# Performance work log

Hardware: AMD Instinct MI355X
Metric: run time of the kernel (lower is better)

Reference implementation:

```python
import jax, jax.numpy as jnp
import numpy as np

# dims
B, T, C, D, H, NH, HD, INTER, L = 4, 1024, 256, 256, 512, 8, 64, 2048, 4
CF, CB, BASE = 0, 128, 10000.0  # context_forward, context_backward, rope theta


def _rope_tables():
    inv = 1.0 / (BASE ** (jnp.arange(0, HD, 2, dtype=jnp.float32) / HD))
    t = jnp.arange(T, dtype=jnp.float32)
    f = jnp.einsum('i,j->ij', t, inv)          # [T, HD/2]
    emb = jnp.concatenate([f, f], axis=-1)      # [T, HD]
    return jnp.cos(emb), jnp.sin(emb)


def _rotate_half(x):
    x1, x2 = jnp.split(x, 2, axis=-1)
    return jnp.concatenate([-x2, x1], axis=-1)


def _ln(x, g, b):
    m = x.mean(-1, keepdims=True)
    v = ((x - m) ** 2).mean(-1, keepdims=True)
    return (x - m) / jnp.sqrt(v + 1e-5) * g + b


def _band_mask():
    # create_context_mask(CF, CB, T): allow j in [i-CB, i+CF]
    i = jnp.arange(T)[:, None]
    j = jnp.arange(T)[None, :]
    return (j <= i + CF) & (j >= i - CB)  # [T, T] bool


def setup_inputs() -> dict:
    key = jax.random.key(0)
    ks = jax.random.split(key, 16)
    w = lambda k, shp: (0.02 * jax.random.normal(k, shp)).astype(jnp.float32)
    return {
        'spikes': jax.random.normal(ks[0], (B, T, C), dtype=jnp.float32),
        'spikes_mask': jnp.ones((B, T), dtype=jnp.int32),
        'spikes_timestamp': jnp.tile(jnp.arange(T, dtype=jnp.int32), (B, 1)),
        'embed_w': w(ks[1], (C, D)), 'embed_b': jnp.zeros((D,), jnp.float32),
        'proj_w': w(ks[2], (D, H)), 'proj_b': jnp.zeros((H,), jnp.float32),
        'ln1_g': jnp.ones((L, H), jnp.float32), 'ln1_b': jnp.zeros((L, H), jnp.float32),
        'Wq': w(ks[3], (L, H, H)), 'bq': jnp.zeros((L, H), jnp.float32),
        'Wk': w(ks[4], (L, H, H)), 'bk': jnp.zeros((L, H), jnp.float32),
        'Wv': w(ks[5], (L, H, H)), 'bv': jnp.zeros((L, H), jnp.float32),
        'Wo': w(ks[6], (L, H, H)), 'bo': jnp.zeros((L, H), jnp.float32),
        'ln2_g': jnp.ones((L, H), jnp.float32), 'ln2_b': jnp.zeros((L, H), jnp.float32),
        'up_w': w(ks[7], (L, H, INTER)), 'up_b': jnp.zeros((L, INTER), jnp.float32),
        'down_w': w(ks[8], (L, INTER, H)), 'down_b': jnp.zeros((L, H), jnp.float32),
    }


def reference(spikes, spikes_mask, spikes_timestamp, embed_w, embed_b, proj_w, proj_b,
              ln1_g, ln1_b, Wq, bq, Wk, bk, Wv, bv, Wo, bo, ln2_g, ln2_b,
              up_w, up_b, down_w, down_b):
    cos, sin = _rope_tables()
    mask = _band_mask()[None, None] & (spikes_mask[:, None, None, :] > 0)  # [B,1,T,T]
    cs = cos[spikes_timestamp][:, None]  # [B,1,T,HD]
    sn = sin[spikes_timestamp][:, None]
    neg = jnp.finfo(jnp.float32).min

    # NeuralEmbeddingLayer (no stack/pos/tokens): Linear -> gelu -> Linear
    x = jax.nn.gelu(spikes @ embed_w + embed_b, approximate=False) @ proj_w + proj_b

    for l in range(L):
        h = _ln(x, ln1_g[l], ln1_b[l])
        q = (h @ Wq[l] + bq[l]).reshape(B, T, NH, HD).transpose(0, 2, 1, 3)
        k = (h @ Wk[l] + bk[l]).reshape(B, T, NH, HD).transpose(0, 2, 1, 3)
        v = (h @ Wv[l] + bv[l]).reshape(B, T, NH, HD).transpose(0, 2, 1, 3)
        q = q * cs + _rotate_half(q) * sn
        k = k * cs + _rotate_half(k) * sn
        s = jnp.einsum('bhqd,bhkd->bhqk', q, k) / np.float32(np.sqrt(HD))
        s = jnp.where(mask, s, neg)
        p = jax.nn.softmax(s, axis=-1)
        o = jnp.einsum('bhqk,bhkd->bhqd', p, v).transpose(0, 2, 1, 3).reshape(B, T, H)
        x = x + o @ Wo[l] + bo[l]
        h = _ln(x, ln2_g[l], ln2_b[l])
        x = x + jax.nn.gelu(h @ up_w[l] + up_b[l], approximate=False) @ down_w[l] + down_b[l]
    return x
```

## Files before the change

### kernel.cpp

```cpp
#include <hip/hip_runtime.h>
#include <math.h>

#define B_ 4
#define T_ 1024
#define C_ 256
#define D_ 256
#define H_ 512
#define NH_ 8
#define HD_ 64
#define INTER_ 2048
#define L_ 4
#define CB_ 128

typedef short bf16x8 __attribute__((ext_vector_type(8)));
typedef unsigned short ush8 __attribute__((ext_vector_type(8)));
typedef float f32x4 __attribute__((ext_vector_type(4)));

__device__ __forceinline__ float gelu_exact(float x) {
    return 0.5f * x * (1.0f + erff(x * 0.70710678118654752f));
}

__device__ __forceinline__ unsigned short f2bf(float f) {
    unsigned u = __float_as_uint(f);
    u += 0x7fffu + ((u >> 16) & 1u);
    return (unsigned short)(u >> 16);
}
__device__ __forceinline__ float bf2f(unsigned short h) {
    return __uint_as_float((unsigned)h << 16);
}

__device__ __forceinline__ void xcd_swz(int& bx, int& by) {
    const int gx  = gridDim.x;
    const int nwg = gx * gridDim.y;
    int bid = blockIdx.y * gx + blockIdx.x;
    bid = (bid & 7) * (nwg >> 3) + (bid >> 3);
    bx = bid % gx;
    by = bid / gx;
}

template<int ACT, int RES, int OBF, int SPLIT>
__global__ __launch_bounds__(256) void mm64_k(
    const unsigned short* __restrict__ A, const unsigned short* __restrict__ BT,
    const float* __restrict__ b0, const float* __restrict__ b1,
    const float* __restrict__ b2,
    const float* res,
    void* o0, void* o1, void* o2,
    const int M, const int N, const int K)
{
    __shared__ unsigned short As[2][64 * 64];
    __shared__ unsigned short Bs[2][64 * 64];

    int bx, by; xcd_swz(bx, by);

    const int tid  = threadIdx.x;
    const int lane = tid & 63;
    const int w    = tid >> 6;
    const int m0   = by * 64;
    const int n0   = bx * 64;
    const int wm   = (w >> 1) * 32;
    const int wn   = (w & 1) * 32;
    const int l16  = lane & 15;
    const int g16  = lane >> 4;

    f32x4 acc[2][2] = {};

    const unsigned short* Abase = A  + (size_t)m0 * K;
    const unsigned short* Bbase = BT + (size_t)n0 * K;

    const int c0 = (w << 6) + lane;
    const int c1 = c0 + 256;
    const int r0c = c0 >> 3, gk0 = (c0 & 7) ^ (r0c & 7);
    const int r1c = c1 >> 3, gk1 = (c1 & 7) ^ (r1c & 7);

#define STAGE64(buf, kk0) do {                                                                        \
    __builtin_amdgcn_global_load_lds(                                                                 \
        (const __attribute__((address_space(1))) unsigned*)(Abase + (size_t)r0c * K + (kk0) + gk0 * 8), \
        (__attribute__((address_space(3))) unsigned*)(As[buf] + (size_t)(w << 6) * 8), 16, 0, 0);     \
    __builtin_amdgcn_global_load_lds(                                                                 \
        (const __attribute__((address_space(1))) unsigned*)(Abase + (size_t)r1c * K + (kk0) + gk1 * 8), \
        (__attribute__((address_space(3))) unsigned*)(As[buf] + (size_t)(256 + (w << 6)) * 8), 16, 0, 0); \
    __builtin_amdgcn_global_load_lds(                                                                 \
        (const __attribute__((address_space(1))) unsigned*)(Bbase + (size_t)r0c * K + (kk0) + gk0 * 8), \
        (__attribute__((address_space(3))) unsigned*)(Bs[buf] + (size_t)(w << 6) * 8), 16, 0, 0);     \
    __builtin_amdgcn_global_load_lds(                                                                 \
        (const __attribute__((address_space(1))) unsigned*)(Bbase + (size_t)r1c * K + (kk0) + gk1 * 8), \
        (__attribute__((address_space(3))) unsigned*)(Bs[buf] + (size_t)(256 + (w << 6)) * 8), 16, 0, 0); \
} while (0)

    for (int k0 = 0; k0 < K; k0 += 128) {
        __syncthreads();
        STAGE64(0, k0);
        STAGE64(1, k0 + 64);
        __syncthreads();

#pragma unroll
        for (int half = 0; half < 2; ++half) {
#pragma unroll
            for (int kk = 0; kk < 2; ++kk) {
                const int kf = kk * 4 + g16;
                const int sw = (kf ^ (l16 & 7)) * 8;
                bf16x8 a[2], b[2];
#pragma unroll
                for (int t = 0; t < 2; ++t)
                    a[t] = *(const bf16x8*)&As[half][(wm + t * 16 + l16) * 64 + sw];
#pragma unroll
                for (int t = 0; t < 2; ++t)
                    b[t] = *(const bf16x8*)&Bs[half][(wn + t * 16 + l16) * 64 + sw];
#pragma unroll
                for (int i = 0; i < 2; ++i)
#pragma unroll
                    for (int j = 0; j < 2; ++j)
                        acc[i][j] = __builtin_amdgcn_mfma_f32_16x16x32_bf16(a[i], b[j], acc[i][j], 0, 0, 0);
            }
        }
    }
#undef STAGE64

    if (OBF || SPLIT) {
        __syncthreads();
        unsigned short* Eb = ((w < 2) ? As[0] : Bs[0]) + (w & 1) * 1024;
        const int row16 = lane >> 2;
        const int cg    = lane & 3;

        const int gnb   = n0 + wn;
        const int which = SPLIT ? (gnb >> 9) : 0;
        const int lnb   = SPLIT ? (gnb & 511) : gnb;
        const int ldo   = SPLIT ? 512 : N;
        unsigned short* oo = SPLIT
            ? ((which == 0) ? (unsigned short*)o0 : (which == 1) ? (unsigned short*)o1 : (unsigned short*)o2)
            : (unsigned short*)o0;
        const float* bb = SPLIT ? ((which == 0) ? b0 : (which == 1) ? b1 : b2) : b0;
        const float scale = (SPLIT && which == 0) ? 0.125f : 1.0f;

#pragma unroll
        for (int i = 0; i < 2; ++i) {
#pragma unroll
            for (int j = 0; j < 2; ++j) {
                const float bv = bb[lnb + j * 16 + l16];
#pragma unroll
                for (int r = 0; r < 4; ++r) {
                    float cv = acc[i][j][r] + bv;
                    if (ACT) cv = gelu_exact(cv);
                    if (SPLIT) cv *= scale;
                    Eb[(g16 * 4 + r) * 40 + j * 16 + l16] = f2bf(cv);
                }
            }
            const int grow0 = m0 + wm + i * 16 + row16;
#pragma unroll
            for (int s = 0; s < 2; ++s) {
                ushort4 t4 = *(const ushort4*)&Eb[row16 * 40 + s * 16 + cg * 4];
                *(ushort4*)&oo[(size_t)grow0 * ldo + lnb + s * 16 + cg * 4] = t4;
            }
        }
        return;
    }

#pragma unroll
    for (int i = 0; i < 2; ++i) {
        const int gmb = m0 + wm + i * 16 + g16 * 4;
#pragma unroll
        for (int j = 0; j < 2; ++j) {
            const int gn = n0 + wn + j * 16 + l16;
            const float bv = b0[gn];
#pragma unroll
            for (int r = 0; r < 4; ++r) {
                float cv = acc[i][j][r] + bv;
                if (ACT) cv = gelu_exact(cv);
                if (RES) cv += res[(size_t)(gmb + r) * 512 + gn];
                ((float*)o0)[(size_t)(gmb + r) * N + gn] = cv;
            }
        }
    }
}

template<int ACT, int RES, int OBF, int SPLIT>
__global__ __launch_bounds__(256) void mm128_k(
    const unsigned short* __restrict__ A, const unsigned short* __restrict__ BT,
    const float* __restrict__ b0, const float* __restrict__ b1,
    const float* __restrict__ b2,
    const float* res,
    void* o0, void* o1, void* o2,
    const int M, const int N, const int K)
{
    __shared__ unsigned short As[128 * 64];
    __shared__ unsigned short Bs[64 * 64];

    int bx, by; xcd_swz(bx, by);

    const int tid  = threadIdx.x;
    const int lane = tid & 63;
    const int w    = tid >> 6;
    const int m0   = by * 128;
    const int n0   = bx * 64;
    const int wm   = (w >> 1) * 64;
    const int wn   = (w & 1) * 32;
    const int l16  = lane & 15;
    const int g16  = lane >> 4;

    f32x4 acc[4][2] = {};

    const unsigned short* Abase = A  + (size_t)m0 * K;
    const unsigned short* Bbase = BT + (size_t)n0 * K;

    for (int k0 = 0; k0 < K; k0 += 64) {
        __syncthreads();
#pragma unroll
        for (int it = 0; it < 4; ++it) {
            const int c = it * 256 + tid;
            const int rc = c >> 3, gk = (c & 7) ^ (rc & 7);
            __builtin_amdgcn_global_load_lds(
                (const __attribute__((address_space(1))) unsigned*)(Abase + (size_t)rc * K + k0 + gk * 8),
                (__attribute__((address_space(3))) unsigned*)(As + (size_t)(it * 256 + (w << 6)) * 8), 16, 0, 0);
        }
#pragma unroll
        for (int it = 0; it < 2; ++it) {
            const int c = it * 256 + tid;
            const int rc = c >> 3, gk = (c & 7) ^ (rc & 7);
            __builtin_amdgcn_global_load_lds(
                (const __attribute__((address_space(1))) unsigned*)(Bbase + (size_t)rc * K + k0 + gk * 8),
                (__attribute__((address_space(3))) unsigned*)(Bs + (size_t)(it * 256 + (w << 6)) * 8), 16, 0, 0);
        }
        __syncthreads();

#pragma unroll
        for (int kk = 0; kk < 2; ++kk) {
            const int kf = kk * 4 + g16;
            const int sw = (kf ^ (l16 & 7)) * 8;
            bf16x8 a[4], b[2];
#pragma unroll
            for (int t = 0; t < 4; ++t)
                a[t] = *(const bf16x8*)&As[(wm + t * 16 + l16) * 64 + sw];
#pragma unroll
            for (int t = 0; t < 2; ++t)
                b[t] = *(const bf16x8*)&Bs[(wn + t * 16 + l16) * 64 + sw];
#pragma unroll
            for (int i = 0; i < 4; ++i)
#pragma unroll
                for (int j = 0; j < 2; ++j)
                    acc[i][j] = __builtin_amdgcn_mfma_f32_16x16x32_bf16(a[i], b[j], acc[i][j], 0, 0, 0);
        }
    }

    if (OBF || SPLIT) {
        __syncthreads();
        constexpr int EST = 40;
        unsigned short* Eb = As + w * (16 * EST);
        const int erow = lane >> 3;
        const int ecol = (lane & 7) * 4;

        const int gnb   = n0 + wn;
        const int which = SPLIT ? (gnb >> 9) : 0;
        const int lnb   = SPLIT ? (gnb & 511) : gnb;
        const int ldo   = SPLIT ? 512 : N;
        unsigned short* oo = SPLIT
            ? ((which == 0) ? (unsigned short*)o0 : (which == 1) ? (unsigned short*)o1 : (unsigned short*)o2)
            : (unsigned short*)o0;
        const float* bb = SPLIT ? ((which == 0) ? b0 : (which == 1) ? b1 : b2) : b0;
        const float scale = (SPLIT && which == 0) ? 0.125f : 1.0f;

#pragma unroll
        for (int i = 0; i < 4; ++i) {
#pragma unroll
            for (int j = 0; j < 2; ++j) {
                const float bv = bb[lnb + j * 16 + l16];
#pragma unroll
                for (int r = 0; r < 4; ++r) {
                    float cv = acc[i][j][r] + bv;
                    if (ACT) cv = gelu_exact(cv);
                    if (SPLIT) cv *= scale;
                    Eb[(g16 * 4 + r) * EST + j * 16 + l16] = f2bf(cv);
                }
            }
            const int grow0 = m0 + wm + i * 16;
#pragma unroll
            for (int s = 0; s < 2; ++s) {
                ushort4 t4 = *(const ushort4*)&Eb[(s * 8 + erow) * EST + ecol];
                *(ushort4*)&oo[(size_t)(grow0 + s * 8 + erow) * ldo + lnb + ecol] = t4;
            }
        }
        return;
    }

#pragma unroll
    for (int i = 0; i < 4; ++i) {
        const int gmb = m0 + wm + i * 16 + g16 * 4;
#pragma unroll
        for (int j = 0; j < 2; ++j) {
            const int gn = n0 + wn + j * 16 + l16;
            const float bv = b0[gn];
#pragma unroll
            for (int r = 0; r < 4; ++r) {
                float cv = acc[i][j][r] + bv;
                if (ACT) cv = gelu_exact(cv);
                if (RES) cv += res[(size_t)(gmb + r) * 512 + gn];
                ((float*)o0)[(size_t)(gmb + r) * N + gn] = cv;
            }
        }
    }
}

__global__ __launch_bounds__(256) void prep_k(
    const float* __restrict__ spikes,
    const float* __restrict__ embed_w, const float* __restrict__ proj_w,
    const float* __restrict__ Wq, const float* __restrict__ Wk,
    const float* __restrict__ Wv, const float* __restrict__ Wo,
    const float* __restrict__ up_w, const float* __restrict__ down_w,
    unsigned short* __restrict__ spbf,
    unsigned short* __restrict__ embT, unsigned short* __restrict__ projT,
    unsigned short* __restrict__ qkvT, unsigned short* __restrict__ woT,
    unsigned short* __restrict__ upT, unsigned short* __restrict__ downT)
{
    const int idx = blockIdx.x;
    const int tid = threadIdx.x;

    if (idx >= 3120) {
        const int base = (idx - 3120) * 4096 + tid * 16;
#pragma unroll
        for (int s = 0; s < 4; ++s) {
            float4 v = *(const float4*)&spikes[base + s * 4];
            ushort4 o = {f2bf(v.x), f2bf(v.y), f2bf(v.z), f2bf(v.w)};
            *(ushort4*)&spbf[base + s * 4] = o;
        }
        return;
    }

    const float* src; unsigned short* dst; int R, Cc, t;
    if (idx < 16)      { src = embed_w; dst = embT;  R = C_; Cc = D_; t = idx; }
    else if (idx < 48) { src = proj_w;  dst = projT; R = D_; Cc = H_; t = idx - 16; }
    else if (idx < 816) {
        const int j = idx - 48;
        const int wsel = j >> 8;
        const int l = (j & 255) >> 6;
        t = j & 63;
        src = ((wsel == 0) ? Wq : (wsel == 1) ? Wk : Wv) + (size_t)l * H_ * H_;
        dst = qkvT + (size_t)l * 3 * H_ * H_ + (size_t)wsel * H_ * H_;
        R = H_; Cc = H_;
    } else if (idx < 1072) {
        const int j = idx - 816; const int l = j >> 6; t = j & 63;
        src = Wo + (size_t)l * H_ * H_; dst = woT + (size_t)l * H_ * H_;
        R = H_; Cc = H_;
    } else if (idx < 2096) {
        const int j = idx - 1072; const int l = j >> 8; t = j & 255;
        src = up_w + (size_t)l * H_ * INTER_; dst = upT + (size_t)l * INTER_ * H_;
        R = H_; Cc = INTER_;
    } else {
        const int j = idx - 2096; const int l = j >> 8; t = j & 255;
        src = down_w + (size_t)l * INTER_ * H_; dst = downT + (size_t)l * H_ * INTER_;
        R = INTER_; Cc = H_;
    }
    const int ntx = Cc >> 6;
    const int c0 = (t % ntx) * 64, r0 = (t / ntx) * 64;

    __shared__ float tile[64][65];
    const int tr = tid >> 4, tc = (tid & 15) * 4;
#pragma unroll
    for (int i = 0; i < 4; ++i) {
        float4 v = *(const float4*)&src[(size_t)(r0 + tr + i * 16) * Cc + c0 + tc];
        tile[tr + i * 16][tc + 0] = v.x;
        tile[tr + i * 16][tc + 1] = v.y;
        tile[tr + i * 16][tc + 2] = v.z;
        tile[tr + i * 16][tc + 3] = v.w;
    }
    __syncthreads();
#pragma unroll
    for (int i = 0; i < 4; ++i) {
        const int n = tr + i * 16;
        ushort4 o;
        o.x = f2bf(tile[tc + 0][n]);
        o.y = f2bf(tile[tc + 1][n]);
        o.z = f2bf(tile[tc + 2][n]);
        o.w = f2bf(tile[tc + 3][n]);
        *(ushort4*)&dst[(size_t)(c0 + n) * R + r0 + tc] = o;
    }
}

__global__ __launch_bounds__(256) void ln_k(
    const float* __restrict__ x, const float* __restrict__ g,
    const float* __restrict__ b, unsigned short* __restrict__ out)
{
    const int row = blockIdx.x;
    const int tid = threadIdx.x;
    const float* xr = x + (size_t)row * H_;

    float v0 = xr[tid];
    float v1 = xr[tid + 256];

    float s = v0 + v1;
#pragma unroll
    for (int off = 32; off; off >>= 1) s += __shfl_xor(s, off);

    __shared__ float red[4];
    const int wave = tid >> 6;
    if ((tid & 63) == 0) red[wave] = s;
    __syncthreads();
    const float mean = (red[0] + red[1] + red[2] + red[3]) * (1.0f / (float)H_);

    const float d0 = v0 - mean, d1 = v1 - mean;
    float q = d0 * d0 + d1 * d1;
#pragma unroll
    for (int off = 32; off; off >>= 1) q += __shfl_xor(q, off);
    __syncthreads();
    if ((tid & 63) == 0) red[wave] = q;
    __syncthreads();
    const float var = (red[0] + red[1] + red[2] + red[3]) * (1.0f / (float)H_);
    const float rstd = rsqrtf(var + 1e-5f);

    out[(size_t)row * H_ + tid]       = f2bf(d0 * rstd * g[tid] + b[tid]);
    out[(size_t)row * H_ + tid + 256] = f2bf(d1 * rstd * g[tid + 256] + b[tid + 256]);
}

#define AWIN 192
#define AKS 72
#define AVS 200

__global__ __launch_bounds__(256) void attn_k(
    const unsigned short* __restrict__ q, const unsigned short* __restrict__ k,
    const unsigned short* __restrict__ v, const int* __restrict__ smask,
    const int* __restrict__ ts, unsigned short* __restrict__ o)
{
    __shared__ unsigned short Ks[AWIN * AKS];
    __shared__ unsigned short Vt[64 * AVS];
    unsigned short* const Pb = Ks;

    const int blk = blockIdx.x;
    const int qt = blk & 15;
    const int h  = (blk >> 4) & 7;
    const int b  = blk >> 7;
    const int tid  = threadIdx.x;
    const int lane = tid & 63;
    const int w    = tid >> 6;
    const int l16  = lane & 15;
    const int g16  = lane >> 4;

    const int qlo = qt * 64;
    const int klo = (qlo >= CB_) ? (qlo - CB_) : 0;
    const int tb  = b * 1024;

    bf16x8 qa0, qa1;
    {
        const int qrow = w * 16 + l16;
        const unsigned short* gq = q + ((size_t)(tb + qlo + qrow)) * 512 + h * 64;
        ush8 lo = *(const ush8*)&gq[g16 * 8];
        ush8 hi = *(const ush8*)&gq[g16 * 8 + 32];
        const float tstamp = (float)ts[tb + qlo + qrow];
#pragma unroll
        for (int j = 0; j < 8; ++j) {
            const int d = g16 * 8 + j;
            const float freq = __expf(-0.2878231366242558f * (float)d);
            const float ang = tstamp * freq;
            const float cc = __cosf(ang), ss = __sinf(ang);
            const float v1 = bf2f(lo[j]);
            const float v2 = bf2f(hi[j]);
            ((unsigned short*)&qa0)[j] = f2bf(v1 * cc - v2 * ss);
            ((unsigned short*)&qa1)[j] = f2bf(v2 * cc + v1 * ss);
        }
    }

    {
        const unsigned short* gk = k + ((size_t)(tb + klo)) * 512 + h * 64;
        for (int c = tid; c < AWIN * 8; c += 256) {
            const int row = c >> 3, c4 = (c & 7) * 4;
            ushort4 lo = *(const ushort4*)&gk[(size_t)row * 512 + c4];
            ushort4 hi = *(const ushort4*)&gk[(size_t)row * 512 + c4 + 32];
            const float tstamp = (float)ts[tb + klo + row];
            ushort4 olo, ohi;
#pragma unroll
            for (int j2 = 0; j2 < 4; ++j2) {
                const float freq = __expf(-0.2878231366242558f * (float)(c4 + j2));
                const float ang = tstamp * freq;
                const float cc = __cosf(ang), ss = __sinf(ang);
                const float v1 = bf2f(((const unsigned short*)&lo)[j2]);
                const float v2 = bf2f(((const unsigned short*)&hi)[j2]);
                ((unsigned short*)&olo)[j2] = f2bf(v1 * cc - v2 * ss);
                ((unsigned short*)&ohi)[j2] = f2bf(v2 * cc + v1 * ss);
            }
            *(ushort4*)&Ks[row * AKS + c4]      = olo;
            *(ushort4*)&Ks[row * AKS + c4 + 32] = ohi;
        }
    }
    {
        const unsigned short* gv = v + ((size_t)(tb + klo)) * 512 + h * 64;
        for (int c = tid; c < AWIN * 16; c += 256) {
            const int row = c >> 4, c4 = (c & 15) * 4;
            ushort4 vv = *(const ushort4*)&gv[(size_t)row * 512 + c4];
            Vt[(c4 + 0) * AVS + row] = vv.x;
            Vt[(c4 + 1) * AVS + row] = vv.y;
            Vt[(c4 + 2) * AVS + row] = vv.z;
            Vt[(c4 + 3) * AVS + row] = vv.w;
        }
    }
    __syncthreads();

    f32x4 accs[12];
#pragma unroll
    for (int t = 0; t < 12; ++t) {
        const bf16x8 b0 = *(const bf16x8*)&Ks[(t * 16 + l16) * AKS + g16 * 8];
        const bf16x8 b1 = *(const bf16x8*)&Ks[(t * 16 + l16) * AKS + 32 + g16 * 8];
        f32x4 c = {};
        c = __builtin_amdgcn_mfma_f32_16x16x32_bf16(qa0, b0, c, 0, 0, 0);
        c = __builtin_amdgcn_mfma_f32_16x16x32_bf16(qa1, b1, c, 0, 0, 0);
        accs[t] = c;
    }

    bool mk[12];
    int  jj[12];
#pragma unroll
    for (int t = 0; t < 12; ++t) {
        jj[t] = klo + t * 16 + l16;
        mk[t] = smask[tb + jj[t]] > 0;
    }

    float rs[4];
#pragma unroll
    for (int r = 0; r < 4; ++r) {
        const int i = qlo + 16 * w + g16 * 4 + r;
        float mx = -1e30f;
#pragma unroll
        for (int t = 0; t < 12; ++t) {
            const bool val = mk[t] && (jj[t] >= i - CB_) && (jj[t] <= i);
            mx = fmaxf(mx, val ? accs[t][r] : -1e30f);
        }
        mx = fmaxf(mx, __shfl_xor(mx, 1));
        mx = fmaxf(mx, __shfl_xor(mx, 2));
        mx = fmaxf(mx, __shfl_xor(mx, 4));
        mx = fmaxf(mx, __shfl_xor(mx, 8));
        float sum = 0.0f;
#pragma unroll
        for (int t = 0; t < 12; ++t) {
            const bool val = mk[t] && (jj[t] >= i - CB_) && (jj[t] <= i);
            const float p = val ? __expf(accs[t][r] - mx) : 0.0f;
            accs[t][r] = p;
            sum += p;
        }
        sum += __shfl_xor(sum, 1);
        sum += __shfl_xor(sum, 2);
        sum += __shfl_xor(sum, 4);
        sum += __shfl_xor(sum, 8);
        rs[r] = 1.0f / sum;
    }

    __syncthreads();

#pragma unroll
    for (int t = 0; t < 12; ++t)
#pragma unroll
        for (int r = 0; r < 4; ++r)
            Pb[(16 * w + g16 * 4 + r) * AVS + t * 16 + l16] = f2bf(accs[t][r]);

    f32x4 acco[4];
#pragma unroll
    for (int nt = 0; nt < 4; ++nt) {
        f32x4 c = {};
#pragma unroll
        for (int ks = 0; ks < 6; ++ks) {
            const bf16x8 a = *(const bf16x8*)&Pb[(16 * w + l16) * AVS + ks * 32 + g16 * 8];
            const bf16x8 bb = *(const bf16x8*)&Vt[(nt * 16 + l16) * AVS + ks * 32 + g16 * 8];
            c = __builtin_amdgcn_mfma_f32_16x16x32_bf16(a, bb, c, 0, 0, 0);
        }
        acco[nt] = c;
    }

    __syncthreads();
#pragma unroll
    for (int nt = 0; nt < 4; ++nt)
#pragma unroll
        for (int r = 0; r < 4; ++r)
            Pb[(16 * w + g16 * 4 + r) * AVS + nt * 16 + l16] = f2bf(acco[nt][r] * rs[r]);

    const int row16 = lane >> 2, cg = lane & 3;
    const int grow = tb + qlo + 16 * w + row16;
#pragma unroll
    for (int s = 0; s < 4; ++s) {
        ushort4 t4 = *(const ushort4*)&Pb[(16 * w + row16) * AVS + s * 16 + cg * 4];
        *(ushort4*)&o[(size_t)grow * 512 + h * 64 + s * 16 + cg * 4] = t4;
    }
}

extern "C" void kernel_launch(void* const* d_in, const int* in_sizes, int n_in,
                              void* d_out, int out_size, void* d_ws, size_t ws_size,
                              hipStream_t stream)
{
    const float* spikes  = (const float*)d_in[0];
    const int*   smask   = (const int*)d_in[1];
    const int*   ts      = (const int*)d_in[2];
    const float* embed_w = (const float*)d_in[3];
    const float* embed_b = (const float*)d_in[4];
    const float* proj_w  = (const float*)d_in[5];
    const float* proj_b  = (const float*)d_in[6];
    const float* ln1_g   = (const float*)d_in[7];
    const float* ln1_b   = (const float*)d_in[8];
    const float* Wq      = (const float*)d_in[9];
    const float* bq      = (const float*)d_in[10];
    const float* Wk      = (const float*)d_in[11];
    const float* bk      = (const float*)d_in[12];
    const float* Wv      = (const float*)d_in[13];
    const float* bv      = (const float*)d_in[14];
    const float* Wo      = (const float*)d_in[15];
    const float* bo      = (const float*)d_in[16];
    const float* ln2_g   = (const float*)d_in[17];
    const float* ln2_b   = (const float*)d_in[18];
    const float* up_w    = (const float*)d_in[19];
    const float* up_b    = (const float*)d_in[20];
    const float* down_w  = (const float*)d_in[21];
    const float* down_b  = (const float*)d_in[22];

    const int M = B_ * T_;

    char* p = (char*)d_ws;
    float* x = (float*)p;                       p += (size_t)M * H_ * 4;
    unsigned short* qb  = (unsigned short*)p;   p += (size_t)M * H_ * 2;
    unsigned short* kb  = (unsigned short*)p;   p += (size_t)M * H_ * 2;
    unsigned short* vb  = (unsigned short*)p;   p += (size_t)M * H_ * 2;
    unsigned short* hbf = (unsigned short*)p;   p += (size_t)M * H_ * 2;
    unsigned short* obf = (unsigned short*)p;   p += (size_t)M * H_ * 2;
    unsigned short* ibf = (unsigned short*)p;   p += (size_t)M * INTER_ * 2;
    unsigned short* tbf = (unsigned short*)p;   p += (size_t)M * D_ * 2;
    unsigned short* spbf  = (unsigned short*)p; p += (size_t)M * C_ * 2;
    unsigned short* embT  = (unsigned short*)p; p += (size_t)D_ * C_ * 2;
    unsigned short* projT = (unsigned short*)p; p += (size_t)H_ * D_ * 2;
    unsigned short* qkvT  = (unsigned short*)p; p += (size_t)L_ * 3 * H_ * H_ * 2;
    unsigned short* woT   = (unsigned short*)p; p += (size_t)L_ * H_ * H_ * 2;
    unsigned short* upT   = (unsigned short*)p; p += (size_t)L_ * INTER_ * H_ * 2;
    unsigned short* downT = (unsigned short*)p; p += (size_t)L_ * H_ * INTER_ * 2;

    prep_k<<<3376, 256, 0, stream>>>(
        spikes, embed_w, proj_w, Wq, Wk, Wv, Wo, up_w, down_w,
        spbf, embT, projT, qkvT, woT, upT, downT);

    mm64_k<1, 0, 1, 0><<<dim3(D_ / 64, M / 64), 256, 0, stream>>>(
        spbf, embT, embed_b, nullptr, nullptr, nullptr,
        tbf, nullptr, nullptr, M, D_, C_);
    mm64_k<0, 0, 0, 0><<<dim3(H_ / 64, M / 64), 256, 0, stream>>>(
        tbf, projT, proj_b, nullptr, nullptr, nullptr,
        x, nullptr, nullptr, M, H_, D_);

    for (int l = 0; l < L_; ++l) {
        const unsigned short* qkvT_l = qkvT + (size_t)l * 3 * H_ * H_;
        const unsigned short* woT_l  = woT  + (size_t)l * H_ * H_;
        const unsigned short* upT_l  = upT  + (size_t)l * INTER_ * H_;
        const unsigned short* dnT_l  = downT + (size_t)l * H_ * INTER_;

        ln_k<<<M, 256, 0, stream>>>(x, ln1_g + l * H_, ln1_b + l * H_, hbf);

        mm128_k<0, 0, 1, 1><<<dim3((3 * H_) / 64, M / 128), 256, 0, stream>>>(
            hbf, qkvT_l, bq + l * H_, bk + l * H_, bv + l * H_, nullptr,
            qb, kb, vb, M, 3 * H_, H_);

        attn_k<<<B_ * NH_ * (T_ / 64), 256, 0, stream>>>(qb, kb, vb, smask, ts, obf);

        mm64_k<0, 1, 0, 0><<<dim3(H_ / 64, M / 64), 256, 0, stream>>>(
            obf, woT_l, bo + l * H_, nullptr, nullptr, x,
            x, nullptr, nullptr, M, H_, H_);

        ln_k<<<M, 256, 0, stream>>>(x, ln2_g + l * H_, ln2_b + l * H_, hbf);

        mm128_k<1, 0, 1, 0><<<dim3(INTER_ / 64, M / 128), 256, 0, stream>>>(
            hbf, upT_l, up_b + l * INTER_, nullptr, nullptr, nullptr,
            ibf, nullptr, nullptr, M, INTER_, H_);

        float* dst = (l == L_ - 1) ? (float*)d_out : x;
        mm64_k<0, 1, 0, 0><<<dim3(H_ / 64, M / 64), 256, 0, stream>>>(
            ibf, dnT_l, down_b + l * H_, nullptr, nullptr, x,
            dst, nullptr, nullptr, M, H_, INTER_);
    }
}
```

Before: 497.9 us.

## Deepen GEMM K-tiles and widen up-projection N tile to 128

The 64x64 GEMM kernel now stages K=256 per barrier pair instead of two 64-wide halves, and the 128-row GEMM stages K=128 per step, so each tile needs fewer syncthreads/load rounds. The 128-row kernel gains a BN template parameter, and the MLP up-projection uses a 128x128 tile to raise per-block data reuse. The cost is larger LDS footprint (64KB and up to 64KB), which lowers occupancy and leaves no overlap between loading and computing, and the up-projection launches half as many blocks.

```diff
diff --git a/kernel.cpp b/kernel.cpp
--- a/kernel.cpp
+++ b/kernel.cpp
@@ -47,8 +47,8 @@
     void* o0, void* o1, void* o2,
     const int M, const int N, const int K)
 {
-    __shared__ unsigned short As[2][64 * 64];
-    __shared__ unsigned short Bs[2][64 * 64];
+    __shared__ unsigned short As[64 * 256];
+    __shared__ unsigned short Bs[64 * 256];
 
     int bx, by; xcd_swz(bx, by);
 
@@ -67,58 +67,50 @@
     const unsigned short* Abase = A  + (size_t)m0 * K;
     const unsigned short* Bbase = BT + (size_t)n0 * K;
 
-    const int c0 = (w << 6) + lane;
-    const int c1 = c0 + 256;
-    const int r0c = c0 >> 3, gk0 = (c0 & 7) ^ (r0c & 7);
-    const int r1c = c1 >> 3, gk1 = (c1 & 7) ^ (r1c & 7);
-
-#define STAGE64(buf, kk0) do {                                                                        \
-    __builtin_amdgcn_global_load_lds(                                                                 \
-        (const __attribute__((address_space(1))) unsigned*)(Abase + (size_t)r0c * K + (kk0) + gk0 * 8), \
-        (__attribute__((address_space(3))) unsigned*)(As[buf] + (size_t)(w << 6) * 8), 16, 0, 0);     \
-    __builtin_amdgcn_global_load_lds(                                                                 \
-        (const __attribute__((address_space(1))) unsigned*)(Abase + (size_t)r1c * K + (kk0) + gk1 * 8), \
-        (__attribute__((address_space(3))) unsigned*)(As[buf] + (size_t)(256 + (w << 6)) * 8), 16, 0, 0); \
-    __builtin_amdgcn_global_load_lds(                                                                 \
-        (const __attribute__((address_space(1))) unsigned*)(Bbase + (size_t)r0c * K + (kk0) + gk0 * 8), \
-        (__attribute__((address_space(3))) unsigned*)(Bs[buf] + (size_t)(w << 6) * 8), 16, 0, 0);     \
-    __builtin_amdgcn_global_load_lds(                                                                 \
-        (const __attribute__((address_space(1))) unsigned*)(Bbase + (size_t)r1c * K + (kk0) + gk1 * 8), \
-        (__attribute__((address_space(3))) unsigned*)(Bs[buf] + (size_t)(256 + (w << 6)) * 8), 16, 0, 0); \
-} while (0)
-
-    for (int k0 = 0; k0 < K; k0 += 128) {
+    for (int k0 = 0; k0 < K; k0 += 256) {
         __syncthreads();
-        STAGE64(0, k0);
-        STAGE64(1, k0 + 64);
+#pragma unroll
+        for (int it = 0; it < 8; ++it) {
+            const int c  = it * 256 + tid;
+            const int rc = c >> 5;
+            const int gk = (c & 31) ^ (rc & 7);
+            __builtin_amdgcn_global_load_lds(
+                (const __attribute__((address_space(1))) unsigned*)(Abase + (size_t)rc * K + k0 + gk * 8),
+                (__attribute__((address_space(3))) unsigned*)(As + (size_t)(it * 256 + (w << 6)) * 8), 16, 0, 0);
+        }
+#pragma unroll
+        for (int it = 0; it < 8; ++it) {
+            const int c  = it * 256 + tid;
+            const int rc = c >> 5;
+            const int gk = (c & 31) ^ (rc & 7);
+            __builtin_amdgcn_global_load_lds(
+                (const __attribute__((address_space(1))) unsigned*)(Bbase + (size_t)rc * K + k0 + gk * 8),
+                (__attribute__((address_space(3))) unsigned*)(Bs + (size_t)(it * 256 + (w << 6)) * 8), 16, 0, 0);
+        }
         __syncthreads();
 
 #pragma unroll
-        for (int half = 0; half < 2; ++half) {
-#pragma unroll
-            for (int kk = 0; kk < 2; ++kk) {
-                const int kf = kk * 4 + g16;
-                const int sw = (kf ^ (l16 & 7)) * 8;
-                bf16x8 a[2], b[2];
-#pragma unroll
-                for (int t = 0; t < 2; ++t)
-                    a[t] = *(const bf16x8*)&As[half][(wm + t * 16 + l16) * 64 + sw];
-#pragma unroll
-                for (int t = 0; t < 2; ++t)
-                    b[t] = *(const bf16x8*)&Bs[half][(wn + t * 16 + l16) * 64 + sw];
-#pragma unroll
-                for (int i = 0; i < 2; ++i)
-#pragma unroll
-                    for (int j = 0; j < 2; ++j)
-                        acc[i][j] = __builtin_amdgcn_mfma_f32_16x16x32_bf16(a[i], b[j], acc[i][j], 0, 0, 0);
-            }
-        }
-    }
-#undef STAGE64
+        for (int kk = 0; kk < 8; ++kk) {
+            const int kf = kk * 4 + g16;
+            const int sw = (kf ^ (l16 & 7)) * 8;
+            bf16x8 a[2], b[2];
+#pragma unroll
+            for (int t = 0; t < 2; ++t)
+                a[t] = *(const bf16x8*)&As[(wm + t * 16 + l16) * 256 + sw];
+#pragma unroll
+            for (int t = 0; t < 2; ++t)
+                b[t] = *(const bf16x8*)&Bs[(wn + t * 16 + l16) * 256 + sw];
+#pragma unroll
+            for (int i = 0; i < 2; ++i)
+#pragma unroll
+                for (int j = 0; j < 2; ++j)
+                    acc[i][j] = __builtin_amdgcn_mfma_f32_16x16x32_bf16(a[i], b[j], acc[i][j], 0, 0, 0);
+        }
+    }
 
     if (OBF || SPLIT) {
         __syncthreads();
-        unsigned short* Eb = ((w < 2) ? As[0] : Bs[0]) + (w & 1) * 1024;
+        unsigned short* Eb = ((w < 2) ? As : Bs) + (w & 1) * 1024;
         const int row16 = lane >> 2;
         const int cg    = lane & 3;
 
@@ -173,7 +165,7 @@
     }
 }
 
-template<int ACT, int RES, int OBF, int SPLIT>
+template<int ACT, int RES, int OBF, int SPLIT, int BN>
 __global__ __launch_bounds__(256) void mm128_k(
     const unsigned short* __restrict__ A, const unsigned short* __restrict__ BT,
     const float* __restrict__ b0, const float* __restrict__ b1,
@@ -182,8 +174,10 @@
     void* o0, void* o1, void* o2,
     const int M, const int N, const int K)
 {
-    __shared__ unsigned short As[128 * 64];
-    __shared__ unsigned short Bs[64 * 64];
+    constexpr int NJ = BN / 32;
+
+    __shared__ unsigned short As[128 * 128];
+    __shared__ unsigned short Bs[BN * 128];
 
     int bx, by; xcd_swz(bx, by);
 
@@ -191,31 +185,33 @@
     const int lane = tid & 63;
     const int w    = tid >> 6;
     const int m0   = by * 128;
-    const int n0   = bx * 64;
+    const int n0   = bx * BN;
     const int wm   = (w >> 1) * 64;
-    const int wn   = (w & 1) * 32;
+    const int wn   = (w & 1) * (BN / 2);
     const int l16  = lane & 15;
     const int g16  = lane >> 4;
 
-    f32x4 acc[4][2] = {};
+    f32x4 acc[4][NJ] = {};
 
     const unsigned short* Abase = A  + (size_t)m0 * K;
     const unsigned short* Bbase = BT + (size_t)n0 * K;
 
-    for (int k0 = 0; k0 < K; k0 += 64) {
+    for (int k0 = 0; k0 < K; k0 += 128) {
         __syncthreads();
 #pragma unroll
-        for (int it = 0; it < 4; ++it) {
-            const int c = it * 256 + tid;
-            const int rc = c >> 3, gk = (c & 7) ^ (rc & 7);
+        for (int it = 0; it < 8; ++it) {
+            const int c  = it * 256 + tid;
+            const int rc = c >> 4;
+            const int gk = (c & 15) ^ (rc & 7);
             __builtin_amdgcn_global_load_lds(
                 (const __attribute__((address_space(1))) unsigned*)(Abase + (size_t)rc * K + k0 + gk * 8),
                 (__attribute__((address_space(3))) unsigned*)(As + (size_t)(it * 256 + (w << 6)) * 8), 16, 0, 0);
         }
 #pragma unroll
-        for (int it = 0; it < 2; ++it) {
-            const int c = it * 256 + tid;
-            const int rc = c >> 3, gk = (c & 7) ^ (rc & 7);
+        for (int it = 0; it < NJ * 2; ++it) {
+            const int c  = it * 256 + tid;
+            const int rc = c >> 4;
+            const int gk = (c & 15) ^ (rc & 7);
             __builtin_amdgcn_global_load_lds(
                 (const __attribute__((address_space(1))) unsigned*)(Bbase + (size_t)rc * K + k0 + gk * 8),
                 (__attribute__((address_space(3))) unsigned*)(Bs + (size_t)(it * 256 + (w << 6)) * 8), 16, 0, 0);
@@ -223,30 +219,33 @@
         __syncthreads();
 
 #pragma unroll
-        for (int kk = 0; kk < 2; ++kk) {
+        for (int kk = 0; kk < 4; ++kk) {
             const int kf = kk * 4 + g16;
             const int sw = (kf ^ (l16 & 7)) * 8;
-            bf16x8 a[4], b[2];
+            bf16x8 a[4], b[NJ];
 #pragma unroll
             for (int t = 0; t < 4; ++t)
-                a[t] = *(const bf16x8*)&As[(wm + t * 16 + l16) * 64 + sw];
-#pragma unroll
-            for (int t = 0; t < 2; ++t)
-                b[t] = *(const bf16x8*)&Bs[(wn + t * 16 + l16) * 64 + sw];
+                a[t] = *(const bf16x8*)&As[(wm + t * 16 + l16) * 128 + sw];
+#pragma unroll
+            for (int t = 0; t < NJ; ++t)
+                b[t] = *(const bf16x8*)&Bs[(wn + t * 16 + l16) * 128 + sw];
 #pragma unroll
             for (int i = 0; i < 4; ++i)
 #pragma unroll
-                for (int j = 0; j < 2; ++j)
+                for (int j = 0; j < NJ; ++j)
                     acc[i][j] = __builtin_amdgcn_mfma_f32_16x16x32_bf16(a[i], b[j], acc[i][j], 0, 0, 0);
         }
     }
 
     if (OBF || SPLIT) {
         __syncthreads();
-        constexpr int EST = 40;
+        constexpr int WC  = NJ * 16;
+        constexpr int EST = WC + 8;
+        constexpr int LPR = WC / 4;
+        constexpr int RPI = 64 / LPR;
         unsigned short* Eb = As + w * (16 * EST);
-        const int erow = lane >> 3;
-        const int ecol = (lane & 7) * 4;
+        const int erow = lane / LPR;
+        const int ecol = (lane % LPR) * 4;
 
         const int gnb   = n0 + wn;
         const int which = SPLIT ? (gnb >> 9) : 0;
@@ -261,7 +260,7 @@
 #pragma unroll
         for (int i = 0; i < 4; ++i) {
 #pragma unroll
-            for (int j = 0; j < 2; ++j) {
+            for (int j = 0; j < NJ; ++j) {
                 const float bv = bb[lnb + j * 16 + l16];
 #pragma unroll
                 for (int r = 0; r < 4; ++r) {
@@ -273,9 +272,9 @@
             }
             const int grow0 = m0 + wm + i * 16;
 #pragma unroll
-            for (int s = 0; s < 2; ++s) {
-                ushort4 t4 = *(const ushort4*)&Eb[(s * 8 + erow) * EST + ecol];
-                *(ushort4*)&oo[(size_t)(grow0 + s * 8 + erow) * ldo + lnb + ecol] = t4;
+            for (int s = 0; s < NJ; ++s) {
+                ushort4 t4 = *(const ushort4*)&Eb[(s * RPI + erow) * EST + ecol];
+                *(ushort4*)&oo[(size_t)(grow0 + s * RPI + erow) * ldo + lnb + ecol] = t4;
             }
         }
         return;
@@ -285,7 +284,7 @@
     for (int i = 0; i < 4; ++i) {
         const int gmb = m0 + wm + i * 16 + g16 * 4;
 #pragma unroll
-        for (int j = 0; j < 2; ++j) {
+        for (int j = 0; j < NJ; ++j) {
             const int gn = n0 + wn + j * 16 + l16;
             const float bv = b0[gn];
 #pragma unroll
@@ -642,7 +641,7 @@
 
         ln_k<<<M, 256, 0, stream>>>(x, ln1_g + l * H_, ln1_b + l * H_, hbf);
 
-        mm128_k<0, 0, 1, 1><<<dim3((3 * H_) / 64, M / 128), 256, 0, stream>>>(
+        mm128_k<0, 0, 1, 1, 64><<<dim3((3 * H_) / 64, M / 128), 256, 0, stream>>>(
             hbf, qkvT_l, bq + l * H_, bk + l * H_, bv + l * H_, nullptr,
             qb, kb, vb, M, 3 * H_, H_);
 
@@ -654,7 +653,7 @@
 
         ln_k<<<M, 256, 0, stream>>>(x, ln2_g + l * H_, ln2_b + l * H_, hbf);
 
-        mm128_k<1, 0, 1, 0><<<dim3(INTER_ / 64, M / 128), 256, 0, stream>>>(
+        mm128_k<1, 0, 1, 0, 128><<<dim3(INTER_ / 128, M / 128), 256, 0, stream>>>(
             hbf, upT_l, up_b + l * INTER_, nullptr, nullptr, nullptr,
             ibf, nullptr, nullptr, M, INTER_, H_);
 
```

New measurement: 493.8 us. No clear change (-0.8%).
